# Kernel tuning notes

Measured on AMD Instinct MI355X. Metric: run time of the kernel, lower is better.

Reference implementation:

```python
import jax, jax.numpy as jnp
import numpy as np

N_EMBED = 8192
EMBED_DIM = 256


def setup_inputs() -> dict:
    key = jax.random.key(0)
    k1, k2 = jax.random.split(key)
    hidden_states = jax.random.normal(k1, (8, EMBED_DIM, 32, 32), dtype=jnp.float32)
    # original inits uniform(-1/n_e, 1/n_e); scale is irrelevant for correctness testing
    emb_weights = jax.random.uniform(
        k2, (N_EMBED, EMBED_DIM), dtype=jnp.float32,
        minval=-1.0 / N_EMBED, maxval=1.0 / N_EMBED)
    return {"hidden_states": hidden_states, "emb_weights": emb_weights}


def reference(hidden_states, emb_weights):
    # (B,C,H,W) -> (B,H,W,C)
    B, C, H, W = hidden_states.shape
    z = jnp.transpose(hidden_states, (0, 2, 3, 1))
    z_flat = z.reshape(-1, C)  # [B*H*W, C]
    # squared euclidean distance: ||z||^2 + ||e||^2 - 2 z e^T
    dist = (jnp.sum(z_flat ** 2, axis=1, keepdims=True)
            + jnp.sum(emb_weights ** 2, axis=1)
            - 2.0 * jnp.matmul(z_flat, emb_weights.T))  # [N, n_embed]
    min_encoding_indices = jnp.argmin(dist, axis=1)  # [N]
    z_q = emb_weights[min_encoding_indices].reshape(B, H, W, C)
    z_q = jnp.transpose(z_q, (0, 3, 1, 2))  # (B,C,H,W)
    min_encoding_indices = min_encoding_indices.reshape(B, -1)
    return z_q, min_encoding_indices
```

## Files before the change

kernel.cpp:

```cpp
#include <hip/hip_runtime.h>
#include <hip/hip_bf16.h>
#include <math.h>

#define C_DIM 256
#define N_EMB 8192
#define N_Z   8192
#define HWB   1024
#define MBLK  128
#define NSPLIT 8
#define SPLITC (N_EMB / NSPLIT)
#define NT    128
#define NTILES (SPLITC / NT)
#define KC    64
#define NSTEPS (NTILES * 4)
#define CK    32
#define EPS   1.1e-3f
#define ZQ_ELEMS (N_Z * C_DIM)

typedef __attribute__((ext_vector_type(8))) short bf16x8;
typedef __attribute__((ext_vector_type(4))) float f32x4;
typedef unsigned short u16;
typedef unsigned int u32;

__device__ __forceinline__ float sqf(float x) { return __fmul_rn(x, x); }

__device__ __forceinline__ u16 f2bf(float v) {
  __hip_bfloat16 h = __float2bfloat16(v);
  u16 r; __builtin_memcpy(&r, &h, 2); return r;
}

template <int STRIDE>
__device__ float pw_sumsq_256(const float* __restrict__ a) {
  float h[2];
#pragma unroll
  for (int hh = 0; hh < 2; ++hh) {
    const float* p = a + hh * 128 * STRIDE;
    float r0 = sqf(p[0 * STRIDE]), r1 = sqf(p[1 * STRIDE]);
    float r2 = sqf(p[2 * STRIDE]), r3 = sqf(p[3 * STRIDE]);
    float r4 = sqf(p[4 * STRIDE]), r5 = sqf(p[5 * STRIDE]);
    float r6 = sqf(p[6 * STRIDE]), r7 = sqf(p[7 * STRIDE]);
    for (int i = 8; i < 128; i += 8) {
      r0 = __fadd_rn(r0, sqf(p[(i + 0) * STRIDE]));
      r1 = __fadd_rn(r1, sqf(p[(i + 1) * STRIDE]));
      r2 = __fadd_rn(r2, sqf(p[(i + 2) * STRIDE]));
      r3 = __fadd_rn(r3, sqf(p[(i + 3) * STRIDE]));
      r4 = __fadd_rn(r4, sqf(p[(i + 4) * STRIDE]));
      r5 = __fadd_rn(r5, sqf(p[(i + 5) * STRIDE]));
      r6 = __fadd_rn(r6, sqf(p[(i + 6) * STRIDE]));
      r7 = __fadd_rn(r7, sqf(p[(i + 7) * STRIDE]));
    }
    h[hh] = __fadd_rn(__fadd_rn(__fadd_rn(r0, r1), __fadd_rn(r2, r3)),
                      __fadd_rn(__fadd_rn(r4, r5), __fadd_rn(r6, r7)));
  }
  return __fadd_rn(h[0], h[1]);
}

__device__ __forceinline__ float exact_score(const float* __restrict__ zr,
                                             const float* __restrict__ er,
                                             float z2v, float e2v) {
  float d = 0.f;
  for (int k4 = 0; k4 < 64; ++k4) {
    float4 a4 = *(const float4*)(zr + k4 * 4);
    float4 b4 = *(const float4*)(er + k4 * 4);
    d = fmaf(a4.x, b4.x, d); d = fmaf(a4.y, b4.y, d);
    d = fmaf(a4.z, b4.z, d); d = fmaf(a4.w, b4.w, d);
  }
  return __fsub_rn(__fadd_rn(z2v, e2v), __fmul_rn(2.f, d));
}

__global__ void vq_tr(const float* __restrict__ hid, float* __restrict__ zt,
                      u16* __restrict__ zbf) {
  __shared__ float tl[32][33];
  int t = threadIdx.x;
  int tx = t & 31, ty = t >> 5;
  int bb = blockIdx.x >> 8;
  int r = blockIdx.x & 255;
  int cT = r >> 5, hwT = r & 31;
#pragma unroll
  for (int p = 0; p < 4; ++p)
    tl[ty + p * 8][tx] =
        hid[((size_t)bb * C_DIM + cT * 32 + ty + p * 8) * HWB + hwT * 32 + tx];
  __syncthreads();
#pragma unroll
  for (int p = 0; p < 4; ++p) {
    float v = tl[tx][ty + p * 8];
    size_t oi = ((size_t)bb * HWB + hwT * 32 + ty + p * 8) * C_DIM + cT * 32 + tx;
    zt[oi] = v;
    zbf[oi] = f2bf(v);
  }
}

__global__ void vq_norms(const float* __restrict__ zt, const float* __restrict__ emb,
                         float* __restrict__ z2, float* __restrict__ e2,
                         u16* __restrict__ ebf) {
  int t = threadIdx.x, b = blockIdx.x;
  if (b < 32) {
    int r = b * 256 + t;
    e2[r] = pw_sumsq_256<1>(emb + (size_t)r * C_DIM);
    for (int k4 = 0; k4 < 64; ++k4) {
      float4 v = *(const float4*)(emb + (size_t)r * C_DIM + k4 * 4);
      ushort4 o;
      o.x = f2bf(v.x); o.y = f2bf(v.y); o.z = f2bf(v.z); o.w = f2bf(v.w);
      *(ushort4*)(ebf + (size_t)r * C_DIM + k4 * 4) = o;
    }
  } else {
    int n = (b - 32) * 256 + t;
    z2[n] = pw_sumsq_256<1>(zt + (size_t)n * C_DIM);
  }
}

__global__ __launch_bounds__(512) void vq_filter(
    const u16* __restrict__ zbf, const u16* __restrict__ ebf,
    const float* __restrict__ zt, const float* __restrict__ emb,
    const float* __restrict__ z2g, const float* __restrict__ e2g,
    float* __restrict__ cd, int* __restrict__ ci) {
  __shared__ u16 zl[MBLK * KC];
  __shared__ u16 el[NT * KC];
  __shared__ float e2l[SPLITC];
  __shared__ u32 mrow[MBLK];
  __shared__ u16 rcol[MBLK * CK];
  __shared__ int rcnt[MBLK];
  __shared__ int ovfr[16];
  __shared__ int novf;
  __shared__ float wbs[8];
  __shared__ int wis[8];

  int t = threadIdx.x;
  int mb = blockIdx.x >> 3;
  int ns = blockIdx.x & 7;
  int n0z = mb * MBLK;
  int l = t & 63;
  int w = t >> 6;
  int wr = w >> 1, wc = w & 1;

  if (t < MBLK) { rcnt[t] = 0; mrow[t] = 0x7f800000u; }
  if (t == 0) novf = 0;
  for (int i = t; i < SPLITC; i += 512) e2l[i] = e2g[ns * SPLITC + i];

  float z2r[2][4];
#pragma unroll
  for (int rf = 0; rf < 2; ++rf)
#pragma unroll
    for (int r = 0; r < 4; ++r)
      z2r[rf][r] = z2g[n0z + wr * 32 + rf * 16 + (l >> 4) * 4 + r];

  float mpl[2][4];
#pragma unroll
  for (int rf = 0; rf < 2; ++rf)
#pragma unroll
    for (int r = 0; r < 4; ++r) mpl[rf][r] = INFINITY;

  const f32x4 vzero = {0.f, 0.f, 0.f, 0.f};
  const int o0r = t >> 3, o0s = t & 7;
  const int o1r = (t + 512) >> 3, o1s = t & 7;
  const int w0off = o0r * KC + ((o0s ^ (o0r & 7)) << 3);
  const int w1off = o1r * KC + ((o1s ^ (o1r & 7)) << 3);

  uint4 gz0, gz1, ge0, ge1;
  {
    const u16* bz = zbf + (size_t)n0z * C_DIM;
    const u16* be = ebf + (size_t)(ns * SPLITC) * C_DIM;
    gz0 = *(const uint4*)(bz + (size_t)o0r * C_DIM + o0s * 8);
    gz1 = *(const uint4*)(bz + (size_t)o1r * C_DIM + o1s * 8);
    ge0 = *(const uint4*)(be + (size_t)o0r * C_DIM + o0s * 8);
    ge1 = *(const uint4*)(be + (size_t)o1r * C_DIM + o1s * 8);
  }

#pragma unroll 1
  for (int pass = 0; pass < 2; ++pass) {
#pragma unroll 1
    for (int tile = 0; tile < NTILES; ++tile) {
      f32x4 acc[2][4];
#pragma unroll
      for (int rf = 0; rf < 2; ++rf)
#pragma unroll
        for (int cf = 0; cf < 4; ++cf) acc[rf][cf] = vzero;

#pragma unroll 1
      for (int kcs = 0; kcs < 4; ++kcs) {
        int stG = pass * NSTEPS + tile * 4 + kcs;
        __syncthreads();
        *(uint4*)(zl + w0off) = gz0;
        *(uint4*)(zl + w1off) = gz1;
        *(uint4*)(el + w0off) = ge0;
        *(uint4*)(el + w1off) = ge1;
        if (stG + 1 < 2 * NSTEPS) {
          int ps = (stG + 1) & (NSTEPS - 1);
          int kc = (ps & 3) * KC;
          int ne0 = ns * SPLITC + (ps >> 2) * NT;
          const u16* bz = zbf + (size_t)n0z * C_DIM + kc;
          const u16* be = ebf + (size_t)ne0 * C_DIM + kc;
          gz0 = *(const uint4*)(bz + (size_t)o0r * C_DIM + o0s * 8);
          gz1 = *(const uint4*)(bz + (size_t)o1r * C_DIM + o1s * 8);
          ge0 = *(const uint4*)(be + (size_t)o0r * C_DIM + o0s * 8);
          ge1 = *(const uint4*)(be + (size_t)o1r * C_DIM + o1s * 8);
        }
        __syncthreads();
#pragma unroll
        for (int ks = 0; ks < 2; ++ks) {
          int so = ((ks * 4 + (l >> 4)) ^ (l & 7)) << 3;
          bf16x8 a0 = *(const bf16x8*)(zl + (wr * 32 + (l & 15)) * KC + so);
          bf16x8 a1 = *(const bf16x8*)(zl + (wr * 32 + 16 + (l & 15)) * KC + so);
#pragma unroll
          for (int cf = 0; cf < 4; ++cf) {
            bf16x8 bfr = *(const bf16x8*)(el + (wc * 64 + cf * 16 + (l & 15)) * KC + so);
            acc[0][cf] = __builtin_amdgcn_mfma_f32_16x16x32_bf16(a0, bfr, acc[0][cf], 0, 0, 0);
            acc[1][cf] = __builtin_amdgcn_mfma_f32_16x16x32_bf16(a1, bfr, acc[1][cf], 0, 0, 0);
          }
        }
      }
      float e2s[4];
#pragma unroll
      for (int cf = 0; cf < 4; ++cf)
        e2s[cf] = e2l[tile * NT + wc * 64 + cf * 16 + (l & 15)];
      if (pass == 0) {
#pragma unroll
        for (int rf = 0; rf < 2; ++rf)
#pragma unroll
          for (int r = 0; r < 4; ++r) {
            float z2v = z2r[rf][r];
            float mn = mpl[rf][r];
#pragma unroll
            for (int cf = 0; cf < 4; ++cf)
              mn = fminf(mn, fmaf(-2.f, acc[rf][cf][r], z2v + e2s[cf]));
            mpl[rf][r] = mn;
          }
      } else {
        int ne0 = ns * SPLITC + tile * NT;
#pragma unroll
        for (int rf = 0; rf < 2; ++rf)
#pragma unroll
          for (int r = 0; r < 4; ++r) {
            int rowl = wr * 32 + rf * 16 + (l >> 4) * 4 + r;
            float z2v = z2r[rf][r];
            float thr = mpl[rf][r];
#pragma unroll
            for (int cf = 0; cf < 4; ++cf) {
              float s = fmaf(-2.f, acc[rf][cf][r], z2v + e2s[cf]);
              if (s <= thr) {
                int pos = atomicAdd(&rcnt[rowl], 1);
                if (pos < CK)
                  rcol[rowl * CK + pos] = (u16)(ne0 + wc * 64 + cf * 16 + (l & 15));
              }
            }
          }
      }
    }
    if (pass == 0) {
#pragma unroll
      for (int rf = 0; rf < 2; ++rf)
#pragma unroll
        for (int r = 0; r < 4; ++r) {
          float mn = mpl[rf][r];
#pragma unroll
          for (int m = 1; m < 16; m <<= 1)
            mn = fminf(mn, __shfl_xor(mn, m, 64));
          if ((l & 15) == 0) {
            int rowl = wr * 32 + rf * 16 + (l >> 4) * 4 + r;
            atomicMin(&mrow[rowl], __float_as_uint(mn));
          }
        }
      __syncthreads();
#pragma unroll
      for (int rf = 0; rf < 2; ++rf)
#pragma unroll
        for (int r = 0; r < 4; ++r) {
          int rowl = wr * 32 + rf * 16 + (l >> 4) * 4 + r;
          mpl[rf][r] = __uint_as_float(mrow[rowl]) + EPS;
        }
    }
  }
  __syncthreads();

  {
    int row = t >> 2;
    int cnt = rcnt[row];
    float b = INFINITY; int bi = N_EMB;
    if (cnt <= CK) {
      const float* zr = zt + (size_t)(n0z + row) * C_DIM;
      float z2v = z2g[n0z + row];
      for (int p2 = (t & 3); p2 < cnt; p2 += 4) {
        int col = rcol[row * CK + p2];
        float s = exact_score(zr, emb + (size_t)col * C_DIM, z2v, e2g[col]);
        if (s < b || (s == b && col < bi)) { b = s; bi = col; }
      }
    }
#pragma unroll
    for (int m = 1; m <= 2; m <<= 1) {
      float ob = __shfl_xor(b, m, 64);
      int oi2 = __shfl_xor(bi, m, 64);
      if (ob < b || (ob == b && oi2 < bi)) { b = ob; bi = oi2; }
    }
    if ((t & 3) == 0 && cnt <= CK) {
      cd[ns * N_Z + n0z + row] = b;
      ci[ns * N_Z + n0z + row] = bi;
    }
  }

  if (t < MBLK && rcnt[t] > CK) {
    int p = atomicAdd(&novf, 1);
    if (p < 16) ovfr[p] = t;
  }
  __syncthreads();
  int no = min(novf, 16);
  for (int oi = 0; oi < no; ++oi) {
    int row = ovfr[oi];
    const float* zr = zt + (size_t)(n0z + row) * C_DIM;
    float z2v = z2g[n0z + row];
    float b = INFINITY; int bi = N_EMB;
#pragma unroll
    for (int q = 0; q < 2; ++q) {
      int col = ns * SPLITC + t * 2 + q;
      float s = exact_score(zr, emb + (size_t)col * C_DIM, z2v, e2g[col]);
      if (s < b || (s == b && col < bi)) { b = s; bi = col; }
    }
#pragma unroll
    for (int m = 1; m <= 32; m <<= 1) {
      float ob = __shfl_xor(b, m, 64);
      int oi2 = __shfl_xor(bi, m, 64);
      if (ob < b || (ob == b && oi2 < bi)) { b = ob; bi = oi2; }
    }
    if (l == 0) { wbs[w] = b; wis[w] = bi; }
    __syncthreads();
    if (t == 0) {
      for (int w2 = 1; w2 < 8; ++w2)
        if (wbs[w2] < b || (wbs[w2] == b && wis[w2] < bi)) { b = wbs[w2]; bi = wis[w2]; }
      cd[ns * N_Z + n0z + row] = b;
      ci[ns * N_Z + n0z + row] = bi;
    }
    __syncthreads();
  }
}

__global__ void vq_out(const float* __restrict__ emb, const float* __restrict__ cd,
                       const int* __restrict__ ci, float* __restrict__ out) {
  __shared__ int sidx[32];
  int t = threadIdx.x;
  int n0 = blockIdx.x * 32;
  if (t < 32) {
    int n = n0 + t;
    float b = INFINITY;
    int bi = 0;
    for (int ns = 0; ns < NSPLIT; ++ns) {
      float d = cd[ns * N_Z + n];
      int i = ci[ns * N_Z + n];
      if (d < b || (d == b && i < bi)) { b = d; bi = i; }
    }
    sidx[t] = bi;
    out[ZQ_ELEMS + n] = (float)bi;
  }
  __syncthreads();
  int bb = n0 >> 10, hw0 = n0 & 1023;
  int nl = t & 31, cg = t >> 5;
#pragma unroll
  for (int p = 0; p < 8; ++p) {
    int c0 = cg * 4 + p * 32;
    float4 v = *(const float4*)(emb + (size_t)sidx[nl] * C_DIM + c0);
    out[((size_t)bb * C_DIM + c0 + 0) * HWB + hw0 + nl] = v.x;
    out[((size_t)bb * C_DIM + c0 + 1) * HWB + hw0 + nl] = v.y;
    out[((size_t)bb * C_DIM + c0 + 2) * HWB + hw0 + nl] = v.z;
    out[((size_t)bb * C_DIM + c0 + 3) * HWB + hw0 + nl] = v.w;
  }
}

extern "C" void kernel_launch(void* const* d_in, const int* in_sizes, int n_in,
                              void* d_out, int out_size, void* d_ws, size_t ws_size,
                              hipStream_t stream) {
  const float* hid = (const float*)d_in[0];
  const float* emb = (const float*)d_in[1];
  float* out = (float*)d_out;

  float* zt = (float*)d_ws;
  float* z2 = zt + (size_t)N_Z * C_DIM;
  float* e2 = z2 + N_Z;
  float* cd = e2 + N_EMB;
  int* ci = (int*)(cd + (size_t)NSPLIT * N_Z);
  u16* zbf = (u16*)(ci + (size_t)NSPLIT * N_Z);
  u16* ebf = zbf + (size_t)N_Z * C_DIM;

  vq_tr<<<2048, 256, 0, stream>>>(hid, zt, zbf);
  vq_norms<<<64, 256, 0, stream>>>(zt, emb, z2, e2, ebf);
  vq_filter<<<(N_Z / MBLK) * NSPLIT, 512, 0, stream>>>(zbf, ebf, zt, emb, z2, e2, cd, ci);
  vq_out<<<N_Z / 32, 256, 0, stream>>>(emb, cd, ci, out);
}
```

Measured before the change: 231.3 us.

## Keep Z fragments in registers and double-buffer codebook via direct global-to-LDS loads

Each block now holds its whole 128-row Z tile as bf16 MFMA fragments in registers instead of restaging it through LDS each K step. Codebook tiles are loaded straight into a double-buffered LDS area with global_load_lds, so the next chunk streams in while the current one is multiplied, and there is one barrier per 128-wide K chunk instead of two per 64-wide chunk. The codebook split goes from 8 to 4 slices, so each block covers more columns and the grid shrinks. The extra registers and the much larger LDS footprint may reduce occupancy or cause spills, even with launch_bounds(512,2).

```diff
diff --git a/kernel.cpp b/kernel.cpp
--- a/kernel.cpp
+++ b/kernel.cpp
@@ -7,12 +7,11 @@
 #define N_Z   8192
 #define HWB   1024
 #define MBLK  128
-#define NSPLIT 8
+#define NSPLIT 4
 #define SPLITC (N_EMB / NSPLIT)
 #define NT    128
 #define NTILES (SPLITC / NT)
-#define KC    64
-#define NSTEPS (NTILES * 4)
+#define NCHUNK (NTILES * 2)
 #define CK    32
 #define EPS   1.1e-3f
 #define ZQ_ELEMS (N_Z * C_DIM)
@@ -27,6 +26,12 @@
 __device__ __forceinline__ u16 f2bf(float v) {
   __hip_bfloat16 h = __float2bfloat16(v);
   u16 r; __builtin_memcpy(&r, &h, 2); return r;
+}
+
+__device__ __forceinline__ void g2l16(const u16* g, u16* l) {
+  __builtin_amdgcn_global_load_lds(
+      (const __attribute__((address_space(1))) unsigned int*)(const void*)g,
+      (__attribute__((address_space(3))) unsigned int*)(void*)l, 16, 0, 0);
 }
 
 template <int STRIDE>
@@ -109,13 +114,12 @@
   }
 }
 
-__global__ __launch_bounds__(512) void vq_filter(
+__global__ __launch_bounds__(512, 2) void vq_filter(
     const u16* __restrict__ zbf, const u16* __restrict__ ebf,
     const float* __restrict__ zt, const float* __restrict__ emb,
     const float* __restrict__ z2g, const float* __restrict__ e2g,
     float* __restrict__ cd, int* __restrict__ ci) {
-  __shared__ u16 zl[MBLK * KC];
-  __shared__ u16 el[NT * KC];
+  __shared__ u16 el[2][16384];
   __shared__ float e2l[SPLITC];
   __shared__ u32 mrow[MBLK];
   __shared__ u16 rcol[MBLK * CK];
@@ -126,8 +130,8 @@
   __shared__ int wis[8];
 
   int t = threadIdx.x;
-  int mb = blockIdx.x >> 3;
-  int ns = blockIdx.x & 7;
+  int mb = blockIdx.x >> 2;
+  int ns = blockIdx.x & 3;
   int n0z = mb * MBLK;
   int l = t & 63;
   int w = t >> 6;
@@ -137,6 +141,14 @@
   if (t == 0) novf = 0;
   for (int i = t; i < SPLITC; i += 512) e2l[i] = e2g[ns * SPLITC + i];
 
+  bf16x8 A[2][8];
+#pragma unroll
+  for (int rf = 0; rf < 2; ++rf)
+#pragma unroll
+    for (int f = 0; f < 8; ++f)
+      A[rf][f] = *(const bf16x8*)(zbf +
+          (size_t)(n0z + wr * 32 + rf * 16 + (l & 15)) * C_DIM + f * 32 + ((l >> 4) << 3));
+
   float z2r[2][4];
 #pragma unroll
   for (int rf = 0; rf < 2; ++rf)
@@ -151,21 +163,25 @@
     for (int r = 0; r < 4; ++r) mpl[rf][r] = INFINITY;
 
   const f32x4 vzero = {0.f, 0.f, 0.f, 0.f};
-  const int o0r = t >> 3, o0s = t & 7;
-  const int o1r = (t + 512) >> 3, o1s = t & 7;
-  const int w0off = o0r * KC + ((o0s ^ (o0r & 7)) << 3);
-  const int w1off = o1r * KC + ((o1s ^ (o1r & 7)) << 3);
-
-  uint4 gz0, gz1, ge0, ge1;
-  {
-    const u16* bz = zbf + (size_t)n0z * C_DIM;
-    const u16* be = ebf + (size_t)(ns * SPLITC) * C_DIM;
-    gz0 = *(const uint4*)(bz + (size_t)o0r * C_DIM + o0s * 8);
-    gz1 = *(const uint4*)(bz + (size_t)o1r * C_DIM + o1s * 8);
-    ge0 = *(const uint4*)(be + (size_t)o0r * C_DIM + o0s * 8);
-    ge1 = *(const uint4*)(be + (size_t)o1r * C_DIM + o1s * 8);
-  }
-
+  const u16* esplit = ebf + (size_t)(ns * SPLITC) * C_DIM;
+
+#define STAGE_E(nb_, c_)                                                      \
+  {                                                                           \
+    int tn_ = (c_) >> 1, kcn_ = ((c_) & 1) << 7;                              \
+    const u16* bs_ = esplit + (size_t)(tn_ * NT) * C_DIM + kcn_;              \
+    _Pragma("unroll")                                                         \
+    for (int p_ = 0; p_ < 4; ++p_) {                                          \
+      int o_ = (w * 4 + p_) * 64 + l;                                         \
+      int g2_ = o_ >> 10, rr_ = (o_ >> 3) & 127, p3_ = o_ & 7;                \
+      g2l16(bs_ + (size_t)rr_ * C_DIM + g2_ * 64 + ((p3_ ^ (rr_ & 7)) << 3),  \
+            &el[nb_][(w * 4 + p_) * 512]);                                    \
+    }                                                                         \
+  }
+
+  STAGE_E(0, 0)
+  __syncthreads();
+
+  int cur = 0;
 #pragma unroll 1
   for (int pass = 0; pass < 2; ++pass) {
 #pragma unroll 1
@@ -176,38 +192,24 @@
 #pragma unroll
         for (int cf = 0; cf < 4; ++cf) acc[rf][cf] = vzero;
 
-#pragma unroll 1
-      for (int kcs = 0; kcs < 4; ++kcs) {
-        int stG = pass * NSTEPS + tile * 4 + kcs;
-        __syncthreads();
-        *(uint4*)(zl + w0off) = gz0;
-        *(uint4*)(zl + w1off) = gz1;
-        *(uint4*)(el + w0off) = ge0;
-        *(uint4*)(el + w1off) = ge1;
-        if (stG + 1 < 2 * NSTEPS) {
-          int ps = (stG + 1) & (NSTEPS - 1);
-          int kc = (ps & 3) * KC;
-          int ne0 = ns * SPLITC + (ps >> 2) * NT;
-          const u16* bz = zbf + (size_t)n0z * C_DIM + kc;
-          const u16* be = ebf + (size_t)ne0 * C_DIM + kc;
-          gz0 = *(const uint4*)(bz + (size_t)o0r * C_DIM + o0s * 8);
-          gz1 = *(const uint4*)(bz + (size_t)o1r * C_DIM + o1s * 8);
-          ge0 = *(const uint4*)(be + (size_t)o0r * C_DIM + o0s * 8);
-          ge1 = *(const uint4*)(be + (size_t)o1r * C_DIM + o1s * 8);
+#pragma unroll
+      for (int half = 0; half < 2; ++half) {
+        int c = tile * 2 + half;
+        if (!(pass == 1 && c == NCHUNK - 1)) STAGE_E(cur ^ 1, (c + 1) & (NCHUNK - 1))
+#pragma unroll
+        for (int kf = 0; kf < 4; ++kf) {
+          int g2 = kf >> 1, ks = kf & 1;
+          int phys = (((ks * 4 + (l >> 4)) ^ (l & 7)) << 3);
+#pragma unroll
+          for (int cf = 0; cf < 4; ++cf) {
+            bf16x8 bfr = *(const bf16x8*)(&el[cur][g2 * 8192 +
+                           (wc * 64 + cf * 16 + (l & 15)) * 64 + phys]);
+            acc[0][cf] = __builtin_amdgcn_mfma_f32_16x16x32_bf16(A[0][half * 4 + kf], bfr, acc[0][cf], 0, 0, 0);
+            acc[1][cf] = __builtin_amdgcn_mfma_f32_16x16x32_bf16(A[1][half * 4 + kf], bfr, acc[1][cf], 0, 0, 0);
+          }
         }
         __syncthreads();
-#pragma unroll
-        for (int ks = 0; ks < 2; ++ks) {
-          int so = ((ks * 4 + (l >> 4)) ^ (l & 7)) << 3;
-          bf16x8 a0 = *(const bf16x8*)(zl + (wr * 32 + (l & 15)) * KC + so);
-          bf16x8 a1 = *(const bf16x8*)(zl + (wr * 32 + 16 + (l & 15)) * KC + so);
-#pragma unroll
-          for (int cf = 0; cf < 4; ++cf) {
-            bf16x8 bfr = *(const bf16x8*)(el + (wc * 64 + cf * 16 + (l & 15)) * KC + so);
-            acc[0][cf] = __builtin_amdgcn_mfma_f32_16x16x32_bf16(a0, bfr, acc[0][cf], 0, 0, 0);
-            acc[1][cf] = __builtin_amdgcn_mfma_f32_16x16x32_bf16(a1, bfr, acc[1][cf], 0, 0, 0);
-          }
-        }
+        cur ^= 1;
       }
       float e2s[4];
 #pragma unroll
@@ -309,8 +311,8 @@
     float z2v = z2g[n0z + row];
     float b = INFINITY; int bi = N_EMB;
 #pragma unroll
-    for (int q = 0; q < 2; ++q) {
-      int col = ns * SPLITC + t * 2 + q;
+    for (int q = 0; q < 4; ++q) {
+      int col = ns * SPLITC + t * 4 + q;
       float s = exact_score(zr, emb + (size_t)col * C_DIM, z2v, e2g[col]);
       if (s < b || (s == b && col < bi)) { b = s; bi = col; }
     }
```

After: 219.3 us. 1.05x faster.
